# Performance work log

Measured on AMD Instinct MI355X. Metric: run time of the kernel, lower is better.

Reference implementation:

```python
import jax, jax.numpy as jnp
import numpy as np
from math import sqrt, pi

B, L, H, E = 16, 512, 8, 64
D = 64


def setup_inputs() -> dict:
    key = jax.random.key(0)
    k1, k2, k3, k4, k5 = jax.random.split(key, 5)
    queries = jax.random.normal(k1, (B, L, H, E), dtype=jnp.float32)
    keys = jax.random.normal(k2, (B, L, H, E), dtype=jnp.float32)
    values = jax.random.normal(k3, (B, L, H, D), dtype=jnp.float32)
    sigma = jax.random.normal(k4, (B, L, H), dtype=jnp.float32)
    head_gate_logit = jax.random.normal(k5, (H,), dtype=jnp.float32)
    # TriangularCausalMask: triu(ones, diagonal=1), broadcast over B,H
    attn_mask = jnp.triu(jnp.ones((L, L), dtype=bool), k=1)[None, None, :, :]
    attn_mask = jnp.broadcast_to(attn_mask, (B, 1, L, L))
    return {"queries": queries, "keys": keys, "values": values,
            "sigma": sigma, "head_gate_logit": head_gate_logit,
            "attn_mask": attn_mask}


def reference(queries, keys, values, sigma, head_gate_logit, attn_mask):
    Bq, Lq, Hq, Eq = queries.shape
    scale = 1.0 / sqrt(Eq)
    # scores: [B,H,L,S]
    scores = jnp.einsum('blhe,bshe->bhls', queries, keys)
    scores = jnp.where(attn_mask, -jnp.inf, scores)
    series = jax.nn.softmax(scale * scores, axis=-1)  # dropout p=0 -> identity

    # sigma: [B,L,H] -> [B,H,L]
    sig = jnp.transpose(sigma, (0, 2, 1))
    sig = jax.nn.sigmoid(sig * 5.0) + 1e-05
    sig = jnp.power(3.0, sig) - 1.0          # [B,H,L]
    sig = sig[..., None]                      # [B,H,L,1]

    i = jnp.arange(Lq, dtype=jnp.float32)
    dist = jnp.abs(i[:, None] - i[None, :])   # [L,L] |i-j|
    prior = (1.0 / (sqrt(2.0 * pi) * sig)) * jnp.exp(-(dist ** 2) / (2.0 * sig ** 2))
    prior_norm = prior / (jnp.sum(prior, axis=-1, keepdims=True) + 1e-08)

    gate = jax.nn.sigmoid(head_gate_logit).reshape(1, Hq, 1, 1)
    fused = gate * series + (1.0 - gate) * prior_norm
    fused = fused / (jnp.sum(fused, axis=-1, keepdims=True) + 1e-08)

    V = jnp.einsum('bhls,bshd->blhd', fused, values)
    return V
```

## Files before the change

kernel.cpp:

```cpp
#include <hip/hip_runtime.h>


#define B_ 16
#define L_ 512
#define H_ 8
#define KST 72
#define VST 72
#define WST 36

typedef __attribute__((ext_vector_type(8))) short bf16x8;
typedef __attribute__((ext_vector_type(4))) float f32x4;
union FR { bf16x8 v; unsigned u[4]; uint4 q4; };

static __device__ __forceinline__ unsigned fbits(float x){union{float f;unsigned u;}c;c.f=x;return c.u;}
static __device__ __forceinline__ float tvf(float x){union{unsigned u;float f;}c;c.u=fbits(x)&0xFFFF0000u;return c.f;}
static __device__ __forceinline__ unsigned pk2(float a,float b){return __builtin_amdgcn_perm(fbits(b),fbits(a),0x07060302u);}

static __device__ __forceinline__ void barrier_lgkm(){
  asm volatile("s_waitcnt lgkmcnt(0)" ::: "memory");
  __builtin_amdgcn_s_barrier();
  asm volatile("" ::: "memory");
}

__global__ __launch_bounds__(256,3) void anomaly_attn(
    const float* __restrict__ Q, const float* __restrict__ K,
    const float* __restrict__ V, const float* __restrict__ Sig,
    const float* __restrict__ Gate, float* __restrict__ Out)
{
  __shared__ unsigned short Klds[2][64*KST];
  __shared__ unsigned short Vlds[2][64*VST];
  __shared__ unsigned We[4][16][WST];

  const int tid=threadIdx.x, lane=tid&63, wid=tid>>6, q=lane>>4, c=lane&15;
  const int idx=blockIdx.x, bh=idx&127, t=7-(idx>>7), h=bh&7, b=bh>>3;
  const int l0w = t*64 + wid*16;
  const size_t bh_off = ((size_t)b*L_*H_ + h)*64;
  const float* __restrict__ Qb=Q+bh_off;
  const float* __restrict__ Kb=K+bh_off;
  const float* __restrict__ Vb=V+bh_off;

  const int kr=tid>>2, kcb=tid&3, srp=tid>>3, scb=tid&7;
  const int swz = (c&3)<<3;
  const int gp=(srp>>2)^scb, rpl=srp&3, vb0i=(gp<<3);

  const float* __restrict__ vbase = Vb + (size_t)(2*srp)*512 + scb*8;
  const float* __restrict__ kbase = Kb + (size_t)kr*512 + kcb*16;

  {
    float4 a0=((const float4*)vbase)[0],       a1=((const float4*)vbase)[1];
    float4 b0=((const float4*)(vbase+512))[0], b1=((const float4*)(vbase+512))[1];
    float4 ka=((const float4*)kbase)[0], kb2=((const float4*)kbase)[1];
    float4 kc2=((const float4*)kbase)[2], kd2=((const float4*)kbase)[3];
    ((unsigned*)&Vlds[0][(scb*8+0)*VST+vb0i])[rpl]=pk2(a0.x,b0.x);
    ((unsigned*)&Vlds[0][(scb*8+1)*VST+vb0i])[rpl]=pk2(a0.y,b0.y);
    ((unsigned*)&Vlds[0][(scb*8+2)*VST+vb0i])[rpl]=pk2(a0.z,b0.z);
    ((unsigned*)&Vlds[0][(scb*8+3)*VST+vb0i])[rpl]=pk2(a0.w,b0.w);
    ((unsigned*)&Vlds[0][(scb*8+4)*VST+vb0i])[rpl]=pk2(a1.x,b1.x);
    ((unsigned*)&Vlds[0][(scb*8+5)*VST+vb0i])[rpl]=pk2(a1.y,b1.y);
    ((unsigned*)&Vlds[0][(scb*8+6)*VST+vb0i])[rpl]=pk2(a1.z,b1.z);
    ((unsigned*)&Vlds[0][(scb*8+7)*VST+vb0i])[rpl]=pk2(a1.w,b1.w);
    uint4 w0,w1;
    w0.x=pk2(ka.x,ka.y);   w0.y=pk2(ka.z,ka.w);
    w0.z=pk2(kb2.x,kb2.y); w0.w=pk2(kb2.z,kb2.w);
    w1.x=pk2(kc2.x,kc2.y); w1.y=pk2(kc2.z,kc2.w);
    w1.z=pk2(kd2.x,kd2.y); w1.w=pk2(kd2.z,kd2.w);
    uint4* dst=(uint4*)&Klds[0][kr*KST + kcb*16];
    dst[0]=w0; dst[1]=w1;
  }

  bf16x8 qf[2];
  {
    const float* qrow = Qb + (size_t)(l0w+c)*512;
    #pragma unroll
    for (int ks=0; ks<2; ++ks) {
      const float4 a = *(const float4*)(qrow + ks*32 + q*8);
      const float4 d4 = *(const float4*)(qrow + ks*32 + q*8 + 4);
      FR f;
      f.u[0]=pk2(a.x,a.y);  f.u[1]=pk2(a.z,a.w);
      f.u[2]=pk2(d4.x,d4.y); f.u[3]=pk2(d4.z,d4.w);
      qf[ks]=f.v;
    }
  }

  const float sgv = Sig[((size_t)b*L_ + l0w + c)*H_ + h];
  float sg = 1.f/(1.f+__expf(-5.f*sgv)) + 1e-5f;
  sg = exp2f(sg*1.5849625007211562f) - 1.f;
  const float invs = 0.3989422804014327f/sg;
  const float i2s2 = (0.5f/(sg*sg))*1.44269504088896f;

  float eP=0.f, pP=0.f;
  f32x4 accA[4], accB[4];
  #pragma unroll
  for (int n=0;n<4;++n){accA[n]=(f32x4)0.f;accB[n]=(f32x4)0.f;}

  barrier_lgkm();

  for (int tile=0; tile<8; ++tile) {
    const int s0=tile*64, p=tile&1;
    const unsigned short* __restrict__ Krd=&Klds[p][0];
    const unsigned short* __restrict__ Vrd=&Vlds[p][0];
    const bool live = tile<=t, diag = tile==t;
    const int delta = s0 - l0w;
    const bool bk0 = (delta    >= -95) && (delta    <= 79);
    const bool bk1 = (delta+32 >= -95) && (delta+32 <= 79);

    float4 sva0,sva1,svb0,svb1,ska,skb,skc,skd;
    bool live1=false, vneed1=false;
    if (tile<7) {
      const int d1=delta+64;
      live1 = (tile+1)<=t;
      const bool b0n = (d1    >= -95) && (d1    <= 79);
      const bool b1n = (d1+32 >= -95) && (d1+32 <= 79);
      vneed1 = live1 || b0n || b1n;
      const float* vp = vbase + (size_t)(s0+64)*512;
      const float* kp = kbase + (size_t)(s0+64)*512;
      if (vneed1) {
        sva0=((const float4*)vp)[0];       sva1=((const float4*)vp)[1];
        svb0=((const float4*)(vp+512))[0]; svb1=((const float4*)(vp+512))[1];
      }
      if (live1) {
        ska=((const float4*)kp)[0]; skb=((const float4*)kp)[1];
        skc=((const float4*)kp)[2]; skd=((const float4*)kp)[3];
      }
    }

    int ks2max = -1;
    if (live) {
      const int ntmax = diag ? wid : 3;
      ks2max = diag ? (wid>>1) : 1;
      f32x4 sacc[4];
      #pragma unroll
      for (int nt=0;nt<4;++nt) if (nt<=ntmax) {
        f32x4 s=(f32x4)0.f;
        #pragma unroll
        for (int ks=0;ks<2;++ks){
          const bf16x8 kf=*(const bf16x8*)&Krd[(nt*16+c)*KST + ks*32 + q*8];
          s=__builtin_amdgcn_mfma_f32_16x16x32_bf16(kf,qf[ks],s,0,0,0);
        }
        sacc[nt]=s;
      }
      #pragma unroll
      for (int nt=0;nt<4;++nt) {
        if (nt<=ntmax) {
          float ev[4];
          #pragma unroll
          for (int r=0;r<4;++r) ev[r]=exp2f(sacc[nt][r]*0.180336880110323f);
          if (diag && nt==wid) {
            #pragma unroll
            for (int r=0;r<4;++r) if (4*q+r > c) ev[r]=0.f;
          }
          #pragma unroll
          for (int r=0;r<4;++r) eP += tvf(ev[r]);
          uint2 w; w.x=pk2(ev[0],ev[1]); w.y=pk2(ev[2],ev[3]);
          *(uint2*)&We[wid][c][(nt*8+2*q)^swz]=w;
        } else if (nt <= 2*ks2max+1) {
          uint2 zz; zz.x=0u; zz.y=0u;
          *(uint2*)&We[wid][c][(nt*8+2*q)^swz]=zz;
        }
      }
    }
    asm volatile("s_waitcnt lgkmcnt(0)" ::: "memory");

    FR ef[2], pf[2];
    #pragma unroll
    for (int k2=0;k2<2;++k2){
      if (k2<=ks2max) ef[k2].q4 = *(const uint4*)&We[wid][c][(k2*16+4*q)^swz];
      if (k2 ? bk1 : bk0) {
        float pv[8];
        #pragma unroll
        for (int j=0;j<8;++j){
          const float dd=(float)(c - k2*32 - q*8 - j - delta);
          pv[j]=invs*exp2f(-dd*dd*i2s2);
          pP += tvf(pv[j]);
        }
        pf[k2].u[0]=pk2(pv[0],pv[1]); pf[k2].u[1]=pk2(pv[2],pv[3]);
        pf[k2].u[2]=pk2(pv[4],pv[5]); pf[k2].u[3]=pk2(pv[6],pv[7]);
      }
    }
    #pragma unroll
    for (int nd=0;nd<4;++nd){
      const int d=nd*16+c, dg7=(d>>3)&7;
      #pragma unroll
      for (int k2=0;k2<2;++k2){
        const bool pb = k2 ? bk1 : bk0;
        if (k2<=ks2max || pb) {
          const int g2i=((k2<<2)+q)^dg7;
          const bf16x8 vf=*(const bf16x8*)&Vrd[d*VST + (g2i<<3)];
          if (k2<=ks2max) accA[nd]=__builtin_amdgcn_mfma_f32_16x16x32_bf16(vf,ef[k2].v,accA[nd],0,0,0);
          if (pb)         accB[nd]=__builtin_amdgcn_mfma_f32_16x16x32_bf16(vf,pf[k2].v,accB[nd],0,0,0);
        }
      }
    }

    if (tile<7) {
      const int pn=p^1;
      if (vneed1) {
        ((unsigned*)&Vlds[pn][(scb*8+0)*VST+vb0i])[rpl]=pk2(sva0.x,svb0.x);
        ((unsigned*)&Vlds[pn][(scb*8+1)*VST+vb0i])[rpl]=pk2(sva0.y,svb0.y);
        ((unsigned*)&Vlds[pn][(scb*8+2)*VST+vb0i])[rpl]=pk2(sva0.z,svb0.z);
        ((unsigned*)&Vlds[pn][(scb*8+3)*VST+vb0i])[rpl]=pk2(sva0.w,svb0.w);
        ((unsigned*)&Vlds[pn][(scb*8+4)*VST+vb0i])[rpl]=pk2(sva1.x,svb1.x);
        ((unsigned*)&Vlds[pn][(scb*8+5)*VST+vb0i])[rpl]=pk2(sva1.y,svb1.y);
        ((unsigned*)&Vlds[pn][(scb*8+6)*VST+vb0i])[rpl]=pk2(sva1.z,svb1.z);
        ((unsigned*)&Vlds[pn][(scb*8+7)*VST+vb0i])[rpl]=pk2(sva1.w,svb1.w);
      }
      if (live1) {
        uint4 w0,w1;
        w0.x=pk2(ska.x,ska.y); w0.y=pk2(ska.z,ska.w);
        w0.z=pk2(skb.x,skb.y); w0.w=pk2(skb.z,skb.w);
        w1.x=pk2(skc.x,skc.y); w1.y=pk2(skc.z,skc.w);
        w1.z=pk2(skd.x,skd.y); w1.w=pk2(skd.z,skd.w);
        uint4* dst=(uint4*)&Klds[pn][kr*KST + kcb*16];
        dst[0]=w0; dst[1]=w1;
      }
    }

    barrier_lgkm();
  }

  eP += __shfl_xor(eP,16,64); eP += __shfl_xor(eP,32,64);
  pP += __shfl_xor(pP,16,64); pP += __shfl_xor(pP,32,64);
  float g=Gate[h]; g=1.f/(1.f+__expf(-g));
  const float cA=g/eP;
  const float cB=(1.f-g)/(pP+1e-8f);
  const float Sf=g+(1.f-g)*(pP/(pP+1e-8f));
  const float nf=1.f/(Sf+1e-8f);
  #pragma unroll
  for (int nd=0;nd<4;++nd){
    float4 o;
    o.x=(cA*accA[nd][0]+cB*accB[nd][0])*nf;
    o.y=(cA*accA[nd][1]+cB*accB[nd][1])*nf;
    o.z=(cA*accA[nd][2]+cB*accB[nd][2])*nf;
    o.w=(cA*accA[nd][3]+cB*accB[nd][3])*nf;
    *(float4*)&Out[bh_off + (size_t)(l0w+c)*512 + nd*16 + 4*q] = o;
  }
}

extern "C" void kernel_launch(void* const* d_in, const int* in_sizes, int n_in,
                              void* d_out, int out_size, void* d_ws, size_t ws_size,
                              hipStream_t stream) {
    const float* Q    = (const float*)d_in[0];
    const float* K    = (const float*)d_in[1];
    const float* V    = (const float*)d_in[2];
    const float* Sig  = (const float*)d_in[3];
    const float* Gate = (const float*)d_in[4];
    float* Out = (float*)d_out;

    dim3 grid(8 * B_ * H_);
    anomaly_attn<<<grid, 256, 0, stream>>>(Q, K, V, Sig, Gate, Out);
}
```

Baseline: 124.3 us.

## Feed softmax weights to PV MFMA directly from registers via 16x16x16 bf16

Drops the per-wave LDS staging buffer used to reshape exp-scores from the QK^T output layout into the PV B-operand layout. It switches the PV product to 16x16x16 bf16 MFMA, whose 4-element operand matches the QK^T accumulator layout, so packed exponentials go straight from registers. The Gaussian prior band check also moves to 16-column granularity, which skips more out-of-band work. The cost is twice as many MFMA issues with half the K depth each, plus narrower V LDS reads.

```diff
diff --git a/kernel.cpp b/kernel.cpp
--- a/kernel.cpp
+++ b/kernel.cpp
@@ -6,15 +6,32 @@
 #define H_ 8
 #define KST 72
 #define VST 72
-#define WST 36
 
 typedef __attribute__((ext_vector_type(8))) short bf16x8;
+typedef __attribute__((ext_vector_type(4))) short bf16x4;
 typedef __attribute__((ext_vector_type(4))) float f32x4;
 union FR { bf16x8 v; unsigned u[4]; uint4 q4; };
+union F2 { bf16x4 v; unsigned u[2]; };
 
 static __device__ __forceinline__ unsigned fbits(float x){union{float f;unsigned u;}c;c.f=x;return c.u;}
 static __device__ __forceinline__ float tvf(float x){union{unsigned u;float f;}c;c.u=fbits(x)&0xFFFF0000u;return c.f;}
 static __device__ __forceinline__ unsigned pk2(float a,float b){return __builtin_amdgcn_perm(fbits(b),fbits(a),0x07060302u);}
+
+#if defined(__has_builtin)
+#if __has_builtin(__builtin_amdgcn_mfma_f32_16x16x16bf16_1k)
+#define HAVE_MFMA16 1
+#endif
+#endif
+
+static __device__ __forceinline__ f32x4 mfma16(bf16x4 a, bf16x4 b, f32x4 c){
+#ifdef HAVE_MFMA16
+  return __builtin_amdgcn_mfma_f32_16x16x16bf16_1k(a,b,c,0,0,0);
+#else
+  asm volatile("s_nop 1\n\tv_mfma_f32_16x16x16_bf16 %0, %1, %2, %0"
+               : "+v"(c) : "v"(a), "v"(b));
+  return c;
+#endif
+}
 
 static __device__ __forceinline__ void barrier_lgkm(){
   asm volatile("s_waitcnt lgkmcnt(0)" ::: "memory");
@@ -29,7 +46,6 @@
 {
   __shared__ unsigned short Klds[2][64*KST];
   __shared__ unsigned short Vlds[2][64*VST];
-  __shared__ unsigned We[4][16][WST];
 
   const int tid=threadIdx.x, lane=tid&63, wid=tid>>6, q=lane>>4, c=lane&15;
   const int idx=blockIdx.x, bh=idx&127, t=7-(idx>>7), h=bh&7, b=bh>>3;
@@ -40,7 +56,6 @@
   const float* __restrict__ Vb=V+bh_off;
 
   const int kr=tid>>2, kcb=tid&3, srp=tid>>3, scb=tid&7;
-  const int swz = (c&3)<<3;
   const int gp=(srp>>2)^scb, rpl=srp&3, vb0i=(gp<<3);
 
   const float* __restrict__ vbase = Vb + (size_t)(2*srp)*512 + scb*8;
@@ -95,14 +110,14 @@
 
   barrier_lgkm();
 
+  const int qh=q>>1, ql=(q&1)<<2;
+
   for (int tile=0; tile<8; ++tile) {
     const int s0=tile*64, p=tile&1;
     const unsigned short* __restrict__ Krd=&Klds[p][0];
     const unsigned short* __restrict__ Vrd=&Vlds[p][0];
     const bool live = tile<=t, diag = tile==t;
     const int delta = s0 - l0w;
-    const bool bk0 = (delta    >= -95) && (delta    <= 79);
-    const bool bk1 = (delta+32 >= -95) && (delta+32 <= 79);
 
     float4 sva0,sva1,svb0,svb1,ska,skb,skc,skd;
     bool live1=false, vneed1=false;
@@ -123,11 +138,12 @@
         skc=((const float4*)kp)[2]; skd=((const float4*)kp)[3];
       }
     }
-
-    int ks2max = -1;
+    asm volatile("" ::: "memory");
+
+    int ntmax = -1;
+    F2 efv[4];
     if (live) {
-      const int ntmax = diag ? wid : 3;
-      ks2max = diag ? (wid>>1) : 1;
+      ntmax = diag ? wid : 3;
       f32x4 sacc[4];
       #pragma unroll
       for (int nt=0;nt<4;++nt) if (nt<=ntmax) {
@@ -140,54 +156,44 @@
         sacc[nt]=s;
       }
       #pragma unroll
-      for (int nt=0;nt<4;++nt) {
-        if (nt<=ntmax) {
-          float ev[4];
+      for (int nt=0;nt<4;++nt) if (nt<=ntmax) {
+        float ev[4];
+        #pragma unroll
+        for (int r=0;r<4;++r) ev[r]=exp2f(sacc[nt][r]*0.180336880110323f);
+        if (diag && nt==wid) {
           #pragma unroll
-          for (int r=0;r<4;++r) ev[r]=exp2f(sacc[nt][r]*0.180336880110323f);
-          if (diag && nt==wid) {
-            #pragma unroll
-            for (int r=0;r<4;++r) if (4*q+r > c) ev[r]=0.f;
+          for (int r=0;r<4;++r) if (4*q+r > c) ev[r]=0.f;
+        }
+        #pragma unroll
+        for (int r=0;r<4;++r) eP += tvf(ev[r]);
+        efv[nt].u[0]=pk2(ev[0],ev[1]); efv[nt].u[1]=pk2(ev[2],ev[3]);
+      }
+    }
+
+    #pragma unroll
+    for (int nt=0;nt<4;++nt) {
+      const bool ea = live && (nt<=ntmax);
+      const int dw = delta + nt*16;
+      const bool pa = (dw >= -79) && (dw <= 79);
+      if (ea || pa) {
+        F2 pfv;
+        if (pa) {
+          float pv[4];
+          #pragma unroll
+          for (int j=0;j<4;++j){
+            const float dd=(float)(c - nt*16 - q*4 - j - delta);
+            pv[j]=invs*exp2f(-dd*dd*i2s2);
+            pP += tvf(pv[j]);
           }
-          #pragma unroll
-          for (int r=0;r<4;++r) eP += tvf(ev[r]);
-          uint2 w; w.x=pk2(ev[0],ev[1]); w.y=pk2(ev[2],ev[3]);
-          *(uint2*)&We[wid][c][(nt*8+2*q)^swz]=w;
-        } else if (nt <= 2*ks2max+1) {
-          uint2 zz; zz.x=0u; zz.y=0u;
-          *(uint2*)&We[wid][c][(nt*8+2*q)^swz]=zz;
-        }
-      }
-    }
-    asm volatile("s_waitcnt lgkmcnt(0)" ::: "memory");
-
-    FR ef[2], pf[2];
-    #pragma unroll
-    for (int k2=0;k2<2;++k2){
-      if (k2<=ks2max) ef[k2].q4 = *(const uint4*)&We[wid][c][(k2*16+4*q)^swz];
-      if (k2 ? bk1 : bk0) {
-        float pv[8];
-        #pragma unroll
-        for (int j=0;j<8;++j){
-          const float dd=(float)(c - k2*32 - q*8 - j - delta);
-          pv[j]=invs*exp2f(-dd*dd*i2s2);
-          pP += tvf(pv[j]);
-        }
-        pf[k2].u[0]=pk2(pv[0],pv[1]); pf[k2].u[1]=pk2(pv[2],pv[3]);
-        pf[k2].u[2]=pk2(pv[4],pv[5]); pf[k2].u[3]=pk2(pv[6],pv[7]);
-      }
-    }
-    #pragma unroll
-    for (int nd=0;nd<4;++nd){
-      const int d=nd*16+c, dg7=(d>>3)&7;
-      #pragma unroll
-      for (int k2=0;k2<2;++k2){
-        const bool pb = k2 ? bk1 : bk0;
-        if (k2<=ks2max || pb) {
-          const int g2i=((k2<<2)+q)^dg7;
-          const bf16x8 vf=*(const bf16x8*)&Vrd[d*VST + (g2i<<3)];
-          if (k2<=ks2max) accA[nd]=__builtin_amdgcn_mfma_f32_16x16x32_bf16(vf,ef[k2].v,accA[nd],0,0,0);
-          if (pb)         accB[nd]=__builtin_amdgcn_mfma_f32_16x16x32_bf16(vf,pf[k2].v,accB[nd],0,0,0);
+          pfv.u[0]=pk2(pv[0],pv[1]); pfv.u[1]=pk2(pv[2],pv[3]);
+        }
+        #pragma unroll
+        for (int nd=0;nd<4;++nd){
+          const int d=nd*16+c;
+          const int graw=(2*nt+qh)^(d>>3);
+          const bf16x4 vf=*(const bf16x4*)&Vrd[d*VST + (graw<<3) + ql];
+          if (ea) accA[nd]=mfma16(vf,efv[nt].v,accA[nd]);
+          if (pa) accB[nd]=mfma16(vf,pfv.v,accB[nd]);
         }
       }
     }
```

Result: slower. 374.2 us (+201.0%).

## Feed softmax scores straight from registers into 16x16x16 MFMA for PV

Applied to the files above, without the earlier changes.

When the 16x16x16 bf16 MFMA builtin is available, the exp'd score tile produced by the QK^T MFMA is packed in registers and used directly as the B operand of 16x16x16 MFMAs for the PV product. This removes the LDS round-trip through the We buffer and its wait. The Gaussian prior term is also computed per 16-column chunk with a tighter band test. The cost is twice as many smaller MFMA instructions and narrower 8-byte V loads from LDS.

```diff
diff --git a/kernel.cpp b/kernel.cpp
--- a/kernel.cpp
+++ b/kernel.cpp
@@ -9,12 +9,26 @@
 #define WST 36
 
 typedef __attribute__((ext_vector_type(8))) short bf16x8;
+typedef __attribute__((ext_vector_type(4))) short bf16x4;
 typedef __attribute__((ext_vector_type(4))) float f32x4;
 union FR { bf16x8 v; unsigned u[4]; uint4 q4; };
 
 static __device__ __forceinline__ unsigned fbits(float x){union{float f;unsigned u;}c;c.f=x;return c.u;}
 static __device__ __forceinline__ float tvf(float x){union{unsigned u;float f;}c;c.u=fbits(x)&0xFFFF0000u;return c.f;}
 static __device__ __forceinline__ unsigned pk2(float a,float b){return __builtin_amdgcn_perm(fbits(b),fbits(a),0x07060302u);}
+
+#if defined(__has_builtin)
+#if __has_builtin(__builtin_amdgcn_mfma_f32_16x16x16bf16_1k)
+#define HAVE_MFMA16 1
+#endif
+#endif
+
+#ifdef HAVE_MFMA16
+static __device__ __forceinline__ bf16x4 mk4(unsigned lo, unsigned hi){
+  uint2 t; t.x=lo; t.y=hi;
+  return __builtin_bit_cast(bf16x4, t);
+}
+#endif
 
 static __device__ __forceinline__ void barrier_lgkm(){
   asm volatile("s_waitcnt lgkmcnt(0)" ::: "memory");
@@ -29,7 +43,9 @@
 {
   __shared__ unsigned short Klds[2][64*KST];
   __shared__ unsigned short Vlds[2][64*VST];
+#ifndef HAVE_MFMA16
   __shared__ unsigned We[4][16][WST];
+#endif
 
   const int tid=threadIdx.x, lane=tid&63, wid=tid>>6, q=lane>>4, c=lane&15;
   const int idx=blockIdx.x, bh=idx&127, t=7-(idx>>7), h=bh&7, b=bh>>3;
@@ -40,8 +56,10 @@
   const float* __restrict__ Vb=V+bh_off;
 
   const int kr=tid>>2, kcb=tid&3, srp=tid>>3, scb=tid&7;
+  const int gp=(srp>>2)^scb, rpl=srp&3, vb0i=(gp<<3);
+#ifndef HAVE_MFMA16
   const int swz = (c&3)<<3;
-  const int gp=(srp>>2)^scb, rpl=srp&3, vb0i=(gp<<3);
+#endif
 
   const float* __restrict__ vbase = Vb + (size_t)(2*srp)*512 + scb*8;
   const float* __restrict__ kbase = Kb + (size_t)kr*512 + kcb*16;
@@ -95,6 +113,10 @@
 
   barrier_lgkm();
 
+#ifdef HAVE_MFMA16
+  const int qh=q>>1, ql=(q&1)<<2;
+#endif
+
   for (int tile=0; tile<8; ++tile) {
     const int s0=tile*64, p=tile&1;
     const unsigned short* __restrict__ Krd=&Klds[p][0];
@@ -123,7 +145,66 @@
         skc=((const float4*)kp)[2]; skd=((const float4*)kp)[3];
       }
     }
-
+    asm volatile("" ::: "memory");
+
+#ifdef HAVE_MFMA16
+    int ntmax = -1;
+    unsigned efu[4][2];
+    if (live) {
+      ntmax = diag ? wid : 3;
+      f32x4 sacc[4];
+      #pragma unroll
+      for (int nt=0;nt<4;++nt) if (nt<=ntmax) {
+        f32x4 s=(f32x4)0.f;
+        #pragma unroll
+        for (int ks=0;ks<2;++ks){
+          const bf16x8 kf=*(const bf16x8*)&Krd[(nt*16+c)*KST + ks*32 + q*8];
+          s=__builtin_amdgcn_mfma_f32_16x16x32_bf16(kf,qf[ks],s,0,0,0);
+        }
+        sacc[nt]=s;
+      }
+      #pragma unroll
+      for (int nt=0;nt<4;++nt) if (nt<=ntmax) {
+        float ev[4];
+        #pragma unroll
+        for (int r=0;r<4;++r) ev[r]=exp2f(sacc[nt][r]*0.180336880110323f);
+        if (diag && nt==wid) {
+          #pragma unroll
+          for (int r=0;r<4;++r) if (4*q+r > c) ev[r]=0.f;
+        }
+        #pragma unroll
+        for (int r=0;r<4;++r) eP += tvf(ev[r]);
+        efu[nt][0]=pk2(ev[0],ev[1]); efu[nt][1]=pk2(ev[2],ev[3]);
+      }
+    }
+    #pragma unroll
+    for (int nt=0;nt<4;++nt) {
+      const bool ea = live && (nt<=ntmax);
+      const int dw = delta + nt*16;
+      const bool pa = (dw >= -79) && (dw <= 79);
+      if (ea || pa) {
+        unsigned pf0=0u, pf1=0u;
+        if (pa) {
+          float pv[4];
+          #pragma unroll
+          for (int j=0;j<4;++j){
+            const float dd=(float)(c - nt*16 - q*4 - j - delta);
+            pv[j]=invs*exp2f(-dd*dd*i2s2);
+            pP += tvf(pv[j]);
+          }
+          pf0=pk2(pv[0],pv[1]); pf1=pk2(pv[2],pv[3]);
+        }
+        #pragma unroll
+        for (int nd=0;nd<4;++nd){
+          const int d=nd*16+c;
+          const int graw=(2*nt+qh)^(d>>3);
+          const bf16x4 vf=*(const bf16x4*)&Vrd[d*VST + (graw<<3) + ql];
+          if (ea) accA[nd]=__builtin_amdgcn_mfma_f32_16x16x16bf16_1k(vf,mk4(efu[nt][0],efu[nt][1]),accA[nd],0,0,0);
+          if (pa) accB[nd]=__builtin_amdgcn_mfma_f32_16x16x16bf16_1k(vf,mk4(pf0,pf1),accB[nd],0,0,0);
+        }
+      }
+    }
+#else
     int ks2max = -1;
     if (live) {
       const int ntmax = diag ? wid : 3;
@@ -160,7 +241,6 @@
       }
     }
     asm volatile("s_waitcnt lgkmcnt(0)" ::: "memory");
-
     FR ef[2], pf[2];
     #pragma unroll
     for (int k2=0;k2<2;++k2){
@@ -191,6 +271,7 @@
         }
       }
     }
+#endif
 
     if (tile<7) {
       const int pn=p^1;
```

Result: slower. 192.8 us (+55.1%).
